# Kernel tuning notes

Hardware: AMD Instinct MI355X
Metric: run time of the kernel (lower is better)

The kernel has to match this reference:

```python
import jax, jax.numpy as jnp
import numpy as np

HIDDEN = 2048
N_HEADS = 32
N_KV = 8
HEAD_DIM = 64
B, S = 2, 2048
EPS = 1e-6
ROT_BASE = 10000.0


def _rms_norm(x, w):
    var = jnp.mean(x * x, axis=-1, keepdims=True)
    return x * jax.lax.rsqrt(var + EPS) * w


def _rotate_half(x):
    h = x.shape[-1] // 2
    return jnp.concatenate([-x[..., h:], x[..., :h]], axis=-1)


def _apply_rope(x, cos, sin):
    # x: [B,S,H,D], cos/sin: [S,D] -> broadcast over batch and heads
    c = cos[None, :, None, :]
    s = sin[None, :, None, :]
    return x * c + _rotate_half(x) * s


def setup_inputs() -> dict:
    key = jax.random.key(0)
    ks = jax.random.split(key, 12)
    sd = 0.02
    hidden_states = jax.random.normal(ks[0], (B, S, HIDDEN), dtype=jnp.float32)
    Wq = jax.random.normal(ks[1], (HIDDEN, N_HEADS * HEAD_DIM), dtype=jnp.float32) * sd
    bq = jnp.zeros((N_HEADS * HEAD_DIM,), dtype=jnp.float32)
    Wk = jax.random.normal(ks[2], (HIDDEN, N_KV * HEAD_DIM), dtype=jnp.float32) * sd
    bk = jnp.zeros((N_KV * HEAD_DIM,), dtype=jnp.float32)
    Wv = jax.random.normal(ks[3], (HIDDEN, N_KV * HEAD_DIM), dtype=jnp.float32) * sd
    bv = jnp.zeros((N_KV * HEAD_DIM,), dtype=jnp.float32)
    Wo = jax.random.normal(ks[4], (N_HEADS * HEAD_DIM, HIDDEN), dtype=jnp.float32) * sd
    bo = jnp.zeros((HIDDEN,), dtype=jnp.float32)
    qn_w = jnp.ones((HEAD_DIM,), dtype=jnp.float32)
    kn_w = jnp.ones((HEAD_DIM,), dtype=jnp.float32)
    # rotary tables (Llama convention: duplicated half-dim freqs)
    inv_freq = 1.0 / (ROT_BASE ** (np.arange(0, HEAD_DIM, 2, dtype=np.float32) / HEAD_DIM))
    t = np.arange(S, dtype=np.float32)
    freqs = np.outer(t, inv_freq)              # [S, D/2]
    emb = np.concatenate([freqs, freqs], axis=-1)  # [S, D]
    cos = jnp.asarray(np.cos(emb), dtype=jnp.float32)
    sin = jnp.asarray(np.sin(emb), dtype=jnp.float32)
    cu_seqlens = jnp.asarray([0, S, 2 * S], dtype=jnp.int32)
    return {"hidden_states": hidden_states, "Wq": Wq, "bq": bq, "Wk": Wk, "bk": bk,
            "Wv": Wv, "bv": bv, "Wo": Wo, "bo": bo, "qn_w": qn_w, "kn_w": kn_w,
            "cos": cos, "sin": sin, "cu_seqlens": cu_seqlens, "max_s": S}


def reference(hidden_states, Wq, bq, Wk, bk, Wv, bv, Wo, bo, qn_w, kn_w, cos, sin, cu_seqlens, max_s):
    b, s, _ = hidden_states.shape
    q = (hidden_states @ Wq + bq).reshape(b, s, N_HEADS, HEAD_DIM)
    k = (hidden_states @ Wk + bk).reshape(b, s, N_KV, HEAD_DIM)
    v = (hidden_states @ Wv + bv).reshape(b, s, N_KV, HEAD_DIM)
    q = _rms_norm(q, qn_w)
    k = _rms_norm(k, kn_w)
    q = _apply_rope(q, cos, sin)
    k = _apply_rope(k, cos, sin)
    # GQA: repeat_interleave kv heads to match query heads
    n_rep = N_HEADS // N_KV
    k = jnp.repeat(k, n_rep, axis=2)
    v = jnp.repeat(v, n_rep, axis=2)
    q = q.transpose(0, 2, 1, 3)  # [B,H,S,D]
    k = k.transpose(0, 2, 1, 3)
    v = v.transpose(0, 2, 1, 3)
    scale = 1.0 / jnp.sqrt(jnp.asarray(HEAD_DIM, dtype=q.dtype))
    scores = jnp.einsum("bhqd,bhkd->bhqk", q, k) * scale
    neg = jnp.finfo(scores.dtype).min
    causal = jnp.triu(jnp.ones((s, s), dtype=scores.dtype), k=1)  # [S,S]
    scores = scores + causal[None, None] * neg
    attn = jax.nn.softmax(scores, axis=-1)
    out = jnp.einsum("bhqk,bhkd->bhqd", attn, v)
    out = out.transpose(0, 2, 1, 3).reshape(b, s, N_HEADS * HEAD_DIM)
    return out @ Wo + bo
```

## Files before the change

kernel.cpp:

```cpp
#include <hip/hip_runtime.h>

typedef unsigned short u16;
typedef __attribute__((ext_vector_type(4))) float f32x4;
typedef __attribute__((ext_vector_type(16))) float f32x16;
typedef __attribute__((ext_vector_type(8))) short s16x8;
typedef __attribute__((ext_vector_type(8))) unsigned short u16x8;
typedef __attribute__((ext_vector_type(4))) unsigned short u16x4;

__device__ __forceinline__ float bf2f(u16 u) {
    union { unsigned int i; float f; } x; x.i = ((unsigned int)u) << 16; return x.f;
}
__device__ __forceinline__ u16 f2bf(float f) {
    union { float f; unsigned int i; } x; x.f = f;
    unsigned int r = x.i + 0x7FFFu + ((x.i >> 16) & 1u);
    return (u16)(r >> 16);
}
__device__ __forceinline__ void gload16(const void* g, void* l) {
    __builtin_amdgcn_global_load_lds((const __attribute__((address_space(1))) void*)g,
                                     (__attribute__((address_space(3))) void*)l, 16, 0, 0);
}
__device__ __forceinline__ unsigned cvtpk(float lo, float hi) {
    unsigned r;
    asm("v_cvt_pk_bf16_f32 %0, %1, %2" : "=v"(r) : "v"(lo), "v"(hi));
    return r;
}

#define BATCH 2
#define SEQ 2048
#define HID 2048
#define NH 32
#define NKV 8
#define HD 64
#define TOK (BATCH * SEQ)
#define NQKV 3072
#define QSCALE 0.18033688011112042f

__global__ void k_f32_to_bf16(const float* __restrict__ src, u16* __restrict__ dst, int n4) {
    int i = blockIdx.x * blockDim.x + threadIdx.x;
    if (i >= n4) return;
    f32x4 v = ((const f32x4*)src)[i];
    u16x4 o;
    o[0] = f2bf(v[0]); o[1] = f2bf(v[1]); o[2] = f2bf(v[2]); o[3] = f2bf(v[3]);
    *(u16x4*)(dst + (size_t)i * 4) = o;
}

__global__ void k_transpose_bf16(const float* __restrict__ src, u16* __restrict__ dst, int K, int N) {
    __shared__ float tile[32][33];
    int n0 = blockIdx.x * 32, k0 = blockIdx.y * 32;
    int tx = threadIdx.x, ty = threadIdx.y;
#pragma unroll
    for (int i = 0; i < 4; i++)
        tile[ty + i * 8][tx] = src[(size_t)(k0 + ty + i * 8) * N + n0 + tx];
    __syncthreads();
#pragma unroll
    for (int i = 0; i < 4; i++) {
        int n = n0 + ty + i * 8;
        dst[(size_t)n * K + k0 + tx] = f2bf(tile[tx][ty + i * 8]);
    }
}

__global__ void k_transpose_v(const u16* __restrict__ src, u16* __restrict__ dst) {
    __shared__ u16 tile[32][34];
    const u16* s = src + (size_t)blockIdx.z * SEQ * HD;
    u16* d = dst + (size_t)blockIdx.z * SEQ * HD;
    int d0 = blockIdx.x * 32;
    int s0 = blockIdx.y * 32;
    int tx = threadIdx.x, ty = threadIdx.y;
#pragma unroll
    for (int i = 0; i < 4; i++)
        tile[ty + i * 8][tx] = s[(size_t)(s0 + ty + i * 8) * HD + d0 + tx];
    __syncthreads();
#pragma unroll
    for (int i = 0; i < 4; i++)
        d[(size_t)(d0 + ty + i * 8) * SEQ + s0 + tx] = tile[tx][ty + i * 8];
}

__global__ void k_concat_bias(const float* __restrict__ bq, const float* __restrict__ bk,
                              const float* __restrict__ bv, float* __restrict__ out) {
    int i = blockIdx.x * blockDim.x + threadIdx.x;
    if (i >= NQKV) return;
    out[i] = (i < HID) ? bq[i] : (i < HID + 512 ? bk[i - HID] : bv[i - HID - 512]);
}

template <int OUT_BF16>
__global__ __launch_bounds__(256) void k_gemm_bt(const u16* __restrict__ A, const u16* __restrict__ BT,
                                                 const float* __restrict__ bias, void* __restrict__ Cout,
                                                 int M, int N, int K, int lda, int ldb) {
    __shared__ u16 As[128 * 32];
    __shared__ u16 Bs[128 * 32];
    const int t = threadIdx.x;
    const int gx = gridDim.x;
    int bid = blockIdx.y * gx + blockIdx.x;
    const int cpx = (gx * gridDim.y) >> 3;
    bid = (bid & 7) * cpx + (bid >> 3);
    const int brow = (bid / gx) * 128, bcol = (bid % gx) * 128;
    const int wid = t >> 6, lane = t & 63;
    const int wr = (wid >> 1) * 64, wc = (wid & 1) * 64;
    const int lr = lane & 15;
    const int lk = (lane >> 4) * 8;

    const int srow0 = wid * 32 + (lane >> 2);
    const int scol = (lane & 3) * 8;
    const u16* Ag0 = A + (size_t)(brow + srow0) * lda + scol;
    const u16* Ag1 = A + (size_t)(brow + srow0 + 16) * lda + scol;
    const u16* Bg0 = BT + (size_t)(bcol + srow0) * ldb + scol;
    const u16* Bg1 = BT + (size_t)(bcol + srow0 + 16) * ldb + scol;
    u16* Al0 = As + (wid * 2 + 0) * 512;
    u16* Al1 = As + (wid * 2 + 1) * 512;
    u16* Bl0 = Bs + (wid * 2 + 0) * 512;
    u16* Bl1 = Bs + (wid * 2 + 1) * 512;

    f32x4 acc[4][4] = {};
    for (int k0 = 0; k0 < K; k0 += 32) {
        __syncthreads();
        gload16(Ag0 + k0, Al0);
        gload16(Ag1 + k0, Al1);
        gload16(Bg0 + k0, Bl0);
        gload16(Bg1 + k0, Bl1);
        __syncthreads();
        s16x8 af[4], bf[4];
#pragma unroll
        for (int mi = 0; mi < 4; mi++) af[mi] = *(const s16x8*)(As + (wr + mi * 16 + lr) * 32 + lk);
#pragma unroll
        for (int ni = 0; ni < 4; ni++) bf[ni] = *(const s16x8*)(Bs + (wc + ni * 16 + lr) * 32 + lk);
#pragma unroll
        for (int mi = 0; mi < 4; mi++)
#pragma unroll
            for (int ni = 0; ni < 4; ni++)
                acc[mi][ni] = __builtin_amdgcn_mfma_f32_16x16x32_bf16(af[mi], bf[ni], acc[mi][ni], 0, 0, 0);
    }

    const int drow = ((lane >> 4) << 2);
#pragma unroll
    for (int mi = 0; mi < 4; mi++) {
#pragma unroll
        for (int ni = 0; ni < 4; ni++) {
#pragma unroll
            for (int r = 0; r < 4; r++) {
                int row = brow + wr + mi * 16 + drow + r;
                int col = bcol + wc + ni * 16 + lr;
                float v = acc[mi][ni][r] + bias[col];
                if (OUT_BF16) ((u16*)Cout)[(size_t)row * N + col] = f2bf(v);
                else          ((float*)Cout)[(size_t)row * N + col] = v;
            }
        }
    }
}

__global__ __launch_bounds__(64) void k_norm_rope(const float* __restrict__ QKV,
                                                  const float* __restrict__ qn_w, const float* __restrict__ kn_w,
                                                  const float* __restrict__ cosT, const float* __restrict__ sinT,
                                                  u16* __restrict__ Qp, u16* __restrict__ Kp, u16* __restrict__ Vp) {
    int token = blockIdx.x;
    int slot = blockIdx.y;
    int d = threadIdx.x;
    int b = token >> 11, s = token & 2047;
    const float* row = QKV + (size_t)token * NQKV;
    if (slot < 40) {
        bool isq = slot < 32;
        int h = isq ? slot : slot - 32;
        float x = isq ? row[h * HD + d] : row[HID + h * HD + d];
        float ss = x * x;
#pragma unroll
        for (int o = 32; o; o >>= 1) ss += __shfl_xor(ss, o);
        float r = rsqrtf(ss * (1.0f / 64.0f) + 1e-6f);
        float xn = x * r * (isq ? qn_w[d] : kn_w[d]);
        float part = __shfl_xor(xn, 32);
        float sign = (d < 32) ? -1.f : 1.f;
        float o = xn * cosT[s * HD + d] + sign * part * sinT[s * HD + d];
        if (isq) Qp[(((size_t)(b * NH + h) * SEQ + s) * HD) + d] = f2bf(o * QSCALE);
        else     Kp[(((size_t)(b * NKV + h) * SEQ + s) * HD) + d] = f2bf(o);
    } else {
        int h = slot - 40;
        Vp[(((size_t)(b * NKV + h) * SEQ + s) * HD) + d] = f2bf(row[HID + 512 + h * HD + d]);
    }
}

__global__ __launch_bounds__(256) void k_attn_mfma(const u16* __restrict__ Qp, const u16* __restrict__ Kp,
                                                   const u16* __restrict__ VpT, u16* __restrict__ AO) {
    __shared__ u16 K_lds[64 * 64];
    __shared__ u16 VT_lds[64 * 64];
    __shared__ u16 P_lds[4][32][76];
    const int bid = blockIdx.x;
    const int qt = 15 - (bid >> 6);
    const int hh = bid & 63;
    const int b = hh >> 5, h = hh & 31, kvh = h >> 2;
    const int t = threadIdx.x, w = t >> 6, lane = t & 63;
    const int q5 = lane & 31, hi = lane >> 5;
    const int qwb = qt * 128 + w * 32;
    const int q_abs = qwb + q5;

    const u16* Qb = Qp + (size_t)(b * NH + h) * SEQ * HD;
    const u16* Kb = Kp + (size_t)(b * NKV + kvh) * SEQ * HD;
    const u16* Vb = VpT + (size_t)(b * NKV + kvh) * HD * SEQ;

    s16x8 qf0 = *(const s16x8*)(Qb + (size_t)q_abs * HD + 0 * 16 + hi * 8);
    s16x8 qf1 = *(const s16x8*)(Qb + (size_t)q_abs * HD + 1 * 16 + hi * 8);
    s16x8 qf2 = *(const s16x8*)(Qb + (size_t)q_abs * HD + 2 * 16 + hi * 8);
    s16x8 qf3 = *(const s16x8*)(Qb + (size_t)q_abs * HD + 3 * 16 + hi * 8);

    f32x16 O0, O1;
#pragma unroll
    for (int r = 0; r < 16; r++) { O0[r] = 0.f; O1[r] = 0.f; }
    float m = -1e30f, l = 0.f;

    const int swz = (q5 & 7) << 4;
    const int nkt = 2 * (qt + 1);
    for (int kt = 0; kt < nkt; kt++) {
        const int k0 = kt * 64;
        __syncthreads();
#pragma unroll
        for (int i = 0; i < 2; i++) {
            int c = (w * 2 + i) * 64 + lane;
            int row = c >> 3, gslot = (c & 7) ^ (row & 7);
            gload16(Kb + (size_t)(k0 + row) * HD + gslot * 8, (char*)K_lds + (size_t)(w * 2 + i) * 1024);
            gload16(Vb + (size_t)row * SEQ + k0 + gslot * 8, (char*)VT_lds + (size_t)(w * 2 + i) * 1024);
        }
        __syncthreads();
        if (k0 > qwb + 31) continue;

        f32x16 s0, s1;
#pragma unroll
        for (int r = 0; r < 16; r++) { s0[r] = 0.f; s1[r] = 0.f; }
        __builtin_amdgcn_s_setprio(1);
#pragma unroll
        for (int dblk = 0; dblk < 4; dblk++) {
            s16x8 kf0 = *(const s16x8*)((const char*)K_lds + q5 * 128 + ((dblk * 32 + hi * 16) ^ swz));
            s16x8 kf1 = *(const s16x8*)((const char*)K_lds + (32 + q5) * 128 + ((dblk * 32 + hi * 16) ^ swz));
            s16x8 qq = (dblk == 0) ? qf0 : (dblk == 1) ? qf1 : (dblk == 2) ? qf2 : qf3;
            s0 = __builtin_amdgcn_mfma_f32_32x32x16_bf16(kf0, qq, s0, 0, 0, 0);
            s1 = __builtin_amdgcn_mfma_f32_32x32x16_bf16(kf1, qq, s1, 0, 0, 0);
        }
        __builtin_amdgcn_s_setprio(0);

        if (k0 + 63 > qwb) {
            const int qrel = q_abs - k0;
#pragma unroll
            for (int r = 0; r < 16; r++) {
                int kr = (r & 3) + 8 * (r >> 2) + 4 * hi;
                if (kr > qrel) s0[r] = -1e30f;
                if (kr + 32 > qrel) s1[r] = -1e30f;
            }
        }

        float mt = -1e30f;
#pragma unroll
        for (int r = 0; r < 16; r++) { mt = fmaxf(mt, s0[r]); mt = fmaxf(mt, s1[r]); }
        mt = fmaxf(mt, __shfl_xor(mt, 32));
        if (!__all(mt <= m + 8.0f)) {
            float mn = fmaxf(m, mt);
            float f = exp2f(m - mn);
            l *= f;
#pragma unroll
            for (int r = 0; r < 16; r++) { O0[r] *= f; O1[r] *= f; }
            m = mn;
        }
        float ps = 0.f;
#pragma unroll
        for (int r = 0; r < 16; r++) {
            float p0 = exp2f(s0[r] - m);
            float p1 = exp2f(s1[r] - m);
            s0[r] = p0; s1[r] = p1;
            ps += p0 + p1;
        }
        ps += __shfl_xor(ps, 32);
        l += ps;

#pragma unroll
        for (int i = 0; i < 8; i++) {
            int key = 2 * (i & 1) + 8 * (i >> 1) + 4 * hi;
            *(unsigned*)&P_lds[w][q5][key]      = cvtpk(s0[2 * i], s0[2 * i + 1]);
            *(unsigned*)&P_lds[w][q5][key + 32] = cvtpk(s1[2 * i], s1[2 * i + 1]);
        }

        __builtin_amdgcn_s_setprio(1);
#pragma unroll
        for (int ks = 0; ks < 4; ks++) {
            s16x8 pb  = *(const s16x8*)&P_lds[w][q5][ks * 16 + hi * 8];
            s16x8 vf0 = *(const s16x8*)((const char*)VT_lds + q5 * 128 + ((ks * 32 + hi * 16) ^ swz));
            s16x8 vf1 = *(const s16x8*)((const char*)VT_lds + (32 + q5) * 128 + ((ks * 32 + hi * 16) ^ swz));
            O0 = __builtin_amdgcn_mfma_f32_32x32x16_bf16(vf0, pb, O0, 0, 0, 0);
            O1 = __builtin_amdgcn_mfma_f32_32x32x16_bf16(vf1, pb, O1, 0, 0, 0);
        }
        __builtin_amdgcn_s_setprio(0);
    }

    float inv = 1.0f / l;
    u16* orow = AO + (size_t)(b * SEQ + q_abs) * (NH * HD) + h * HD;
#pragma unroll
    for (int db = 0; db < 2; db++) {
#pragma unroll
        for (int g2 = 0; g2 < 4; g2++) {
            u16x4 wv;
#pragma unroll
            for (int i2 = 0; i2 < 4; i2++) {
                float v = (db == 0 ? O0[g2 * 4 + i2] : O1[g2 * 4 + i2]) * inv;
                wv[i2] = f2bf(v);
            }
            *(u16x4*)(orow + db * 32 + g2 * 8 + hi * 4) = wv;
        }
    }
}

extern "C" void kernel_launch(void* const* d_in, const int* in_sizes, int n_in,
                              void* d_out, int out_size, void* d_ws, size_t ws_size,
                              hipStream_t stream) {
    const float* hs   = (const float*)d_in[0];
    const float* Wq   = (const float*)d_in[1];
    const float* bq   = (const float*)d_in[2];
    const float* Wk   = (const float*)d_in[3];
    const float* bk   = (const float*)d_in[4];
    const float* Wv   = (const float*)d_in[5];
    const float* bv   = (const float*)d_in[6];
    const float* Wo   = (const float*)d_in[7];
    const float* bo   = (const float*)d_in[8];
    const float* qn_w = (const float*)d_in[9];
    const float* kn_w = (const float*)d_in[10];
    const float* cosT = (const float*)d_in[11];
    const float* sinT = (const float*)d_in[12];

    char* ws = (char*)d_ws;
    size_t off = 0;
    auto alloc = [&](size_t bytes) { char* p = ws + off; off = (off + bytes + 255) & ~(size_t)255; return p; };
    u16*   Xb    = (u16*)  alloc((size_t)TOK * HID * 2);
    u16*   WTqkv = (u16*)  alloc((size_t)NQKV * HID * 2);
    u16*   WoT   = (u16*)  alloc((size_t)HID * HID * 2);
    float* bqkv  = (float*)alloc((size_t)NQKV * 4);
    float* QKV   = (float*)alloc((size_t)TOK * NQKV * 4);
    u16*   Qp    = (u16*)  alloc((size_t)BATCH * NH * SEQ * HD * 2);
    u16*   Kp    = (u16*)  alloc((size_t)BATCH * NKV * SEQ * HD * 2);
    u16*   Vp    = (u16*)  alloc((size_t)BATCH * NKV * SEQ * HD * 2);
    u16*   VpT   = (u16*)  alloc((size_t)BATCH * NKV * SEQ * HD * 2);
    u16*   AO    = (u16*)  alloc((size_t)TOK * HID * 2);
    (void)ws_size;

    k_f32_to_bf16<<<(TOK * HID / 4 + 255) / 256, 256, 0, stream>>>(hs, Xb, TOK * HID / 4);
    dim3 tb(32, 8);
    k_transpose_bf16<<<dim3(HID / 32, HID / 32), tb, 0, stream>>>(Wq, WTqkv, HID, HID);
    k_transpose_bf16<<<dim3(512 / 32, HID / 32), tb, 0, stream>>>(Wk, WTqkv + (size_t)HID * HID, HID, 512);
    k_transpose_bf16<<<dim3(512 / 32, HID / 32), tb, 0, stream>>>(Wv, WTqkv + (size_t)(HID + 512) * HID, HID, 512);
    k_transpose_bf16<<<dim3(HID / 32, HID / 32), tb, 0, stream>>>(Wo, WoT, HID, HID);
    k_concat_bias<<<(NQKV + 255) / 256, 256, 0, stream>>>(bq, bk, bv, bqkv);
    k_gemm_bt<0><<<dim3(NQKV / 128, TOK / 128), 256, 0, stream>>>(Xb, WTqkv, bqkv, QKV, TOK, NQKV, HID, HID, HID);
    k_norm_rope<<<dim3(TOK, 48), 64, 0, stream>>>(QKV, qn_w, kn_w, cosT, sinT, Qp, Kp, Vp);
    k_transpose_v<<<dim3(HD / 32, SEQ / 32, BATCH * NKV), tb, 0, stream>>>(Vp, VpT);
    k_attn_mfma<<<BATCH * NH * (SEQ / 128), 256, 0, stream>>>(Qp, Kp, VpT, AO);
    k_gemm_bt<0><<<dim3(HID / 128, TOK / 128), 256, 0, stream>>>(AO, WoT, bo, d_out, TOK, HID, HID, HID, HID);
}
```

Before: 269.4 us.

## Double-buffer K/V tiles in attention and emit QKV projection as bf16

The attention kernel now keeps two LDS buffers for K and V^T and prefetches the next key tile with async global-to-LDS loads while the current tile is computed. This cuts one of the two barriers per iteration and hides load latency behind compute. Separately, the QKV GEMM writes bf16 instead of fp32, halving intermediate traffic into the norm/rope kernel. The bf16 rounding happens before the RMS norm, which slightly lowers precision, and the extra LDS buffers may reduce occupancy.

```diff
diff --git a/kernel.cpp b/kernel.cpp
--- a/kernel.cpp
+++ b/kernel.cpp
@@ -147,7 +147,7 @@
     }
 }
 
-__global__ __launch_bounds__(64) void k_norm_rope(const float* __restrict__ QKV,
+__global__ __launch_bounds__(64) void k_norm_rope(const u16* __restrict__ QKV,
                                                   const float* __restrict__ qn_w, const float* __restrict__ kn_w,
                                                   const float* __restrict__ cosT, const float* __restrict__ sinT,
                                                   u16* __restrict__ Qp, u16* __restrict__ Kp, u16* __restrict__ Vp) {
@@ -155,11 +155,11 @@
     int slot = blockIdx.y;
     int d = threadIdx.x;
     int b = token >> 11, s = token & 2047;
-    const float* row = QKV + (size_t)token * NQKV;
+    const u16* row = QKV + (size_t)token * NQKV;
     if (slot < 40) {
         bool isq = slot < 32;
         int h = isq ? slot : slot - 32;
-        float x = isq ? row[h * HD + d] : row[HID + h * HD + d];
+        float x = isq ? bf2f(row[h * HD + d]) : bf2f(row[HID + h * HD + d]);
         float ss = x * x;
 #pragma unroll
         for (int o = 32; o; o >>= 1) ss += __shfl_xor(ss, o);
@@ -172,14 +172,14 @@
         else     Kp[(((size_t)(b * NKV + h) * SEQ + s) * HD) + d] = f2bf(o);
     } else {
         int h = slot - 40;
-        Vp[(((size_t)(b * NKV + h) * SEQ + s) * HD) + d] = f2bf(row[HID + 512 + h * HD + d]);
+        Vp[(((size_t)(b * NKV + h) * SEQ + s) * HD) + d] = row[HID + 512 + h * HD + d];
     }
 }
 
 __global__ __launch_bounds__(256) void k_attn_mfma(const u16* __restrict__ Qp, const u16* __restrict__ Kp,
                                                    const u16* __restrict__ VpT, u16* __restrict__ AO) {
-    __shared__ u16 K_lds[64 * 64];
-    __shared__ u16 VT_lds[64 * 64];
+    __shared__ u16 K_lds[2][64 * 64];
+    __shared__ u16 VT_lds[2][64 * 64];
     __shared__ u16 P_lds[4][32][76];
     const int bid = blockIdx.x;
     const int qt = 15 - (bid >> 6);
@@ -194,6 +194,10 @@
     const u16* Kb = Kp + (size_t)(b * NKV + kvh) * SEQ * HD;
     const u16* Vb = VpT + (size_t)(b * NKV + kvh) * HD * SEQ;
 
+    const int c0 = (w * 2 + 0) * 64 + lane, c1 = (w * 2 + 1) * 64 + lane;
+    const int r0 = c0 >> 3, g0 = (c0 & 7) ^ (r0 & 7);
+    const int r1 = c1 >> 3, g1 = (c1 & 7) ^ (r1 & 7);
+
     s16x8 qf0 = *(const s16x8*)(Qb + (size_t)q_abs * HD + 0 * 16 + hi * 8);
     s16x8 qf1 = *(const s16x8*)(Qb + (size_t)q_abs * HD + 1 * 16 + hi * 8);
     s16x8 qf2 = *(const s16x8*)(Qb + (size_t)q_abs * HD + 2 * 16 + hi * 8);
@@ -206,83 +210,97 @@
 
     const int swz = (q5 & 7) << 4;
     const int nkt = 2 * (qt + 1);
+
+    {
+        gload16(Kb + (size_t)r0 * HD + g0 * 8, (char*)K_lds[0] + (size_t)(w * 2 + 0) * 1024);
+        gload16(Kb + (size_t)r1 * HD + g1 * 8, (char*)K_lds[0] + (size_t)(w * 2 + 1) * 1024);
+        gload16(Vb + (size_t)r0 * SEQ + g0 * 8, (char*)VT_lds[0] + (size_t)(w * 2 + 0) * 1024);
+        gload16(Vb + (size_t)r1 * SEQ + g1 * 8, (char*)VT_lds[0] + (size_t)(w * 2 + 1) * 1024);
+    }
+    __syncthreads();
+
     for (int kt = 0; kt < nkt; kt++) {
         const int k0 = kt * 64;
+        const int cur = kt & 1;
+        if (kt + 1 < nkt) {
+            const int nk0 = k0 + 64;
+            gload16(Kb + (size_t)(nk0 + r0) * HD + g0 * 8, (char*)K_lds[cur ^ 1] + (size_t)(w * 2 + 0) * 1024);
+            gload16(Kb + (size_t)(nk0 + r1) * HD + g1 * 8, (char*)K_lds[cur ^ 1] + (size_t)(w * 2 + 1) * 1024);
+            gload16(Vb + (size_t)r0 * SEQ + nk0 + g0 * 8, (char*)VT_lds[cur ^ 1] + (size_t)(w * 2 + 0) * 1024);
+            gload16(Vb + (size_t)r1 * SEQ + nk0 + g1 * 8, (char*)VT_lds[cur ^ 1] + (size_t)(w * 2 + 1) * 1024);
+        }
+
+        if (k0 <= qwb + 31) {
+            const char* Kc = (const char*)K_lds[cur];
+            const char* Vc = (const char*)VT_lds[cur];
+
+            f32x16 s0, s1;
+#pragma unroll
+            for (int r = 0; r < 16; r++) { s0[r] = 0.f; s1[r] = 0.f; }
+            __builtin_amdgcn_s_setprio(1);
+#pragma unroll
+            for (int dblk = 0; dblk < 4; dblk++) {
+                s16x8 kf0 = *(const s16x8*)(Kc + q5 * 128 + ((dblk * 32 + hi * 16) ^ swz));
+                s16x8 kf1 = *(const s16x8*)(Kc + (32 + q5) * 128 + ((dblk * 32 + hi * 16) ^ swz));
+                s16x8 qq = (dblk == 0) ? qf0 : (dblk == 1) ? qf1 : (dblk == 2) ? qf2 : qf3;
+                s0 = __builtin_amdgcn_mfma_f32_32x32x16_bf16(kf0, qq, s0, 0, 0, 0);
+                s1 = __builtin_amdgcn_mfma_f32_32x32x16_bf16(kf1, qq, s1, 0, 0, 0);
+            }
+            __builtin_amdgcn_s_setprio(0);
+
+            if (k0 + 63 > qwb) {
+                const int qrel = q_abs - k0;
+#pragma unroll
+                for (int r = 0; r < 16; r++) {
+                    int kr = (r & 3) + 8 * (r >> 2) + 4 * hi;
+                    if (kr > qrel) s0[r] = -1e30f;
+                    if (kr + 32 > qrel) s1[r] = -1e30f;
+                }
+            }
+
+            float mt = -1e30f;
+#pragma unroll
+            for (int r = 0; r < 16; r++) { mt = fmaxf(mt, s0[r]); mt = fmaxf(mt, s1[r]); }
+            mt = fmaxf(mt, __shfl_xor(mt, 32));
+            if (!__all(mt <= m + 8.0f)) {
+                float mn = fmaxf(m, mt);
+                float f = exp2f(m - mn);
+                l *= f;
+#pragma unroll
+                for (int r = 0; r < 16; r++) { O0[r] *= f; O1[r] *= f; }
+                m = mn;
+            }
+            float ps = 0.f;
+#pragma unroll
+            for (int r = 0; r < 16; r++) {
+                float p0 = exp2f(s0[r] - m);
+                float p1 = exp2f(s1[r] - m);
+                s0[r] = p0; s1[r] = p1;
+                ps += p0 + p1;
+            }
+            ps += __shfl_xor(ps, 32);
+            l += ps;
+
+#pragma unroll
+            for (int i = 0; i < 8; i++) {
+                int key = 2 * (i & 1) + 8 * (i >> 1) + 4 * hi;
+                *(unsigned*)&P_lds[w][q5][key]      = cvtpk(s0[2 * i], s0[2 * i + 1]);
+                *(unsigned*)&P_lds[w][q5][key + 32] = cvtpk(s1[2 * i], s1[2 * i + 1]);
+            }
+
+            __builtin_amdgcn_s_setprio(1);
+#pragma unroll
+            for (int ks = 0; ks < 4; ks++) {
+                s16x8 pb  = *(const s16x8*)&P_lds[w][q5][ks * 16 + hi * 8];
+                s16x8 vf0 = *(const s16x8*)(Vc + q5 * 128 + ((ks * 32 + hi * 16) ^ swz));
+                s16x8 vf1 = *(const s16x8*)(Vc + (32 + q5) * 128 + ((ks * 32 + hi * 16) ^ swz));
+                O0 = __builtin_amdgcn_mfma_f32_32x32x16_bf16(vf0, pb, O0, 0, 0, 0);
+                O1 = __builtin_amdgcn_mfma_f32_32x32x16_bf16(vf1, pb, O1, 0, 0, 0);
+            }
+            __builtin_amdgcn_s_setprio(0);
+        }
+
         __syncthreads();
-#pragma unroll
-        for (int i = 0; i < 2; i++) {
-            int c = (w * 2 + i) * 64 + lane;
-            int row = c >> 3, gslot = (c & 7) ^ (row & 7);
-            gload16(Kb + (size_t)(k0 + row) * HD + gslot * 8, (char*)K_lds + (size_t)(w * 2 + i) * 1024);
-            gload16(Vb + (size_t)row * SEQ + k0 + gslot * 8, (char*)VT_lds + (size_t)(w * 2 + i) * 1024);
-        }
-        __syncthreads();
-        if (k0 > qwb + 31) continue;
-
-        f32x16 s0, s1;
-#pragma unroll
-        for (int r = 0; r < 16; r++) { s0[r] = 0.f; s1[r] = 0.f; }
-        __builtin_amdgcn_s_setprio(1);
-#pragma unroll
-        for (int dblk = 0; dblk < 4; dblk++) {
-            s16x8 kf0 = *(const s16x8*)((const char*)K_lds + q5 * 128 + ((dblk * 32 + hi * 16) ^ swz));
-            s16x8 kf1 = *(const s16x8*)((const char*)K_lds + (32 + q5) * 128 + ((dblk * 32 + hi * 16) ^ swz));
-            s16x8 qq = (dblk == 0) ? qf0 : (dblk == 1) ? qf1 : (dblk == 2) ? qf2 : qf3;
-            s0 = __builtin_amdgcn_mfma_f32_32x32x16_bf16(kf0, qq, s0, 0, 0, 0);
-            s1 = __builtin_amdgcn_mfma_f32_32x32x16_bf16(kf1, qq, s1, 0, 0, 0);
-        }
-        __builtin_amdgcn_s_setprio(0);
-
-        if (k0 + 63 > qwb) {
-            const int qrel = q_abs - k0;
-#pragma unroll
-            for (int r = 0; r < 16; r++) {
-                int kr = (r & 3) + 8 * (r >> 2) + 4 * hi;
-                if (kr > qrel) s0[r] = -1e30f;
-                if (kr + 32 > qrel) s1[r] = -1e30f;
-            }
-        }
-
-        float mt = -1e30f;
-#pragma unroll
-        for (int r = 0; r < 16; r++) { mt = fmaxf(mt, s0[r]); mt = fmaxf(mt, s1[r]); }
-        mt = fmaxf(mt, __shfl_xor(mt, 32));
-        if (!__all(mt <= m + 8.0f)) {
-            float mn = fmaxf(m, mt);
-            float f = exp2f(m - mn);
-            l *= f;
-#pragma unroll
-            for (int r = 0; r < 16; r++) { O0[r] *= f; O1[r] *= f; }
-            m = mn;
-        }
-        float ps = 0.f;
-#pragma unroll
-        for (int r = 0; r < 16; r++) {
-            float p0 = exp2f(s0[r] - m);
-            float p1 = exp2f(s1[r] - m);
-            s0[r] = p0; s1[r] = p1;
-            ps += p0 + p1;
-        }
-        ps += __shfl_xor(ps, 32);
-        l += ps;
-
-#pragma unroll
-        for (int i = 0; i < 8; i++) {
-            int key = 2 * (i & 1) + 8 * (i >> 1) + 4 * hi;
-            *(unsigned*)&P_lds[w][q5][key]      = cvtpk(s0[2 * i], s0[2 * i + 1]);
-            *(unsigned*)&P_lds[w][q5][key + 32] = cvtpk(s1[2 * i], s1[2 * i + 1]);
-        }
-
-        __builtin_amdgcn_s_setprio(1);
-#pragma unroll
-        for (int ks = 0; ks < 4; ks++) {
-            s16x8 pb  = *(const s16x8*)&P_lds[w][q5][ks * 16 + hi * 8];
-            s16x8 vf0 = *(const s16x8*)((const char*)VT_lds + q5 * 128 + ((ks * 32 + hi * 16) ^ swz));
-            s16x8 vf1 = *(const s16x8*)((const char*)VT_lds + (32 + q5) * 128 + ((ks * 32 + hi * 16) ^ swz));
-            O0 = __builtin_amdgcn_mfma_f32_32x32x16_bf16(vf0, pb, O0, 0, 0, 0);
-            O1 = __builtin_amdgcn_mfma_f32_32x32x16_bf16(vf1, pb, O1, 0, 0, 0);
-        }
-        __builtin_amdgcn_s_setprio(0);
     }
 
     float inv = 1.0f / l;
@@ -326,7 +344,7 @@
     u16*   WTqkv = (u16*)  alloc((size_t)NQKV * HID * 2);
     u16*   WoT   = (u16*)  alloc((size_t)HID * HID * 2);
     float* bqkv  = (float*)alloc((size_t)NQKV * 4);
-    float* QKV   = (float*)alloc((size_t)TOK * NQKV * 4);
+    u16*   QKV   = (u16*)  alloc((size_t)TOK * NQKV * 2);
     u16*   Qp    = (u16*)  alloc((size_t)BATCH * NH * SEQ * HD * 2);
     u16*   Kp    = (u16*)  alloc((size_t)BATCH * NKV * SEQ * HD * 2);
     u16*   Vp    = (u16*)  alloc((size_t)BATCH * NKV * SEQ * HD * 2);
@@ -341,7 +359,7 @@
     k_transpose_bf16<<<dim3(512 / 32, HID / 32), tb, 0, stream>>>(Wv, WTqkv + (size_t)(HID + 512) * HID, HID, 512);
     k_transpose_bf16<<<dim3(HID / 32, HID / 32), tb, 0, stream>>>(Wo, WoT, HID, HID);
     k_concat_bias<<<(NQKV + 255) / 256, 256, 0, stream>>>(bq, bk, bv, bqkv);
-    k_gemm_bt<0><<<dim3(NQKV / 128, TOK / 128), 256, 0, stream>>>(Xb, WTqkv, bqkv, QKV, TOK, NQKV, HID, HID, HID);
+    k_gemm_bt<1><<<dim3(NQKV / 128, TOK / 128), 256, 0, stream>>>(Xb, WTqkv, bqkv, QKV, TOK, NQKV, HID, HID, HID);
     k_norm_rope<<<dim3(TOK, 48), 64, 0, stream>>>(QKV, qn_w, kn_w, cosT, sinT, Qp, Kp, Vp);
     k_transpose_v<<<dim3(HD / 32, SEQ / 32, BATCH * NKV), tb, 0, stream>>>(Vp, VpT);
     k_attn_mfma<<<BATCH * NH * (SEQ / 128), 256, 0, stream>>>(Qp, Kp, VpT, AO);
```

New measurement: 269.9 us. No clear change (+0.2%).

## Emit bf16 QKV from GEMM and load K/V fragments directly from global in attention

Applied to the files above, without the earlier changes.

The QKV projection GEMM now writes bf16 instead of fp32, halving the intermediate write and the read in the norm/rope kernel, and V is copied through without conversion. The attention kernel drops its shared-memory K/V staging and block-wide barriers. Each wave now loads its own K and V MFMA fragments straight from global memory and runs its own causal trip count. This removes synchronisation and lets waves skip fully masked tiles, at the cost of redundant global/L2 traffic across the four waves and exposed load latency without prefetching. Rounding QKV to bf16 before RMS norm also slightly lowers precision.

```diff
diff --git a/kernel.cpp b/kernel.cpp
--- a/kernel.cpp
+++ b/kernel.cpp
@@ -147,7 +147,7 @@
     }
 }
 
-__global__ __launch_bounds__(64) void k_norm_rope(const float* __restrict__ QKV,
+__global__ __launch_bounds__(64) void k_norm_rope(const u16* __restrict__ QKV,
                                                   const float* __restrict__ qn_w, const float* __restrict__ kn_w,
                                                   const float* __restrict__ cosT, const float* __restrict__ sinT,
                                                   u16* __restrict__ Qp, u16* __restrict__ Kp, u16* __restrict__ Vp) {
@@ -155,11 +155,11 @@
     int slot = blockIdx.y;
     int d = threadIdx.x;
     int b = token >> 11, s = token & 2047;
-    const float* row = QKV + (size_t)token * NQKV;
+    const u16* row = QKV + (size_t)token * NQKV;
     if (slot < 40) {
         bool isq = slot < 32;
         int h = isq ? slot : slot - 32;
-        float x = isq ? row[h * HD + d] : row[HID + h * HD + d];
+        float x = isq ? bf2f(row[h * HD + d]) : bf2f(row[HID + h * HD + d]);
         float ss = x * x;
 #pragma unroll
         for (int o = 32; o; o >>= 1) ss += __shfl_xor(ss, o);
@@ -172,14 +172,12 @@
         else     Kp[(((size_t)(b * NKV + h) * SEQ + s) * HD) + d] = f2bf(o);
     } else {
         int h = slot - 40;
-        Vp[(((size_t)(b * NKV + h) * SEQ + s) * HD) + d] = f2bf(row[HID + 512 + h * HD + d]);
+        Vp[(((size_t)(b * NKV + h) * SEQ + s) * HD) + d] = row[HID + 512 + h * HD + d];
     }
 }
 
 __global__ __launch_bounds__(256) void k_attn_mfma(const u16* __restrict__ Qp, const u16* __restrict__ Kp,
                                                    const u16* __restrict__ VpT, u16* __restrict__ AO) {
-    __shared__ u16 K_lds[64 * 64];
-    __shared__ u16 VT_lds[64 * 64];
     __shared__ u16 P_lds[4][32][76];
     const int bid = blockIdx.x;
     const int qt = 15 - (bid >> 6);
@@ -204,20 +202,27 @@
     for (int r = 0; r < 16; r++) { O0[r] = 0.f; O1[r] = 0.f; }
     float m = -1e30f, l = 0.f;
 
-    const int swz = (q5 & 7) << 4;
-    const int nkt = 2 * (qt + 1);
-    for (int kt = 0; kt < nkt; kt++) {
+    const u16* Krow0 = Kb + (size_t)q5 * HD + hi * 8;
+    const u16* Krow1 = Kb + (size_t)(32 + q5) * HD + hi * 8;
+    const u16* Vrow0 = Vb + (size_t)q5 * SEQ + hi * 8;
+    const u16* Vrow1 = Vb + (size_t)(32 + q5) * SEQ + hi * 8;
+
+    const int nkt_w = 2 * qt + 1 + (w >> 1);
+    for (int kt = 0; kt < nkt_w; kt++) {
         const int k0 = kt * 64;
-        __syncthreads();
-#pragma unroll
-        for (int i = 0; i < 2; i++) {
-            int c = (w * 2 + i) * 64 + lane;
-            int row = c >> 3, gslot = (c & 7) ^ (row & 7);
-            gload16(Kb + (size_t)(k0 + row) * HD + gslot * 8, (char*)K_lds + (size_t)(w * 2 + i) * 1024);
-            gload16(Vb + (size_t)row * SEQ + k0 + gslot * 8, (char*)VT_lds + (size_t)(w * 2 + i) * 1024);
-        }
-        __syncthreads();
-        if (k0 > qwb + 31) continue;
+
+        s16x8 kf0[4], kf1[4];
+#pragma unroll
+        for (int dblk = 0; dblk < 4; dblk++) {
+            kf0[dblk] = *(const s16x8*)(Krow0 + (size_t)k0 * HD + dblk * 16);
+            kf1[dblk] = *(const s16x8*)(Krow1 + (size_t)k0 * HD + dblk * 16);
+        }
+        s16x8 vf0[4], vf1[4];
+#pragma unroll
+        for (int ks = 0; ks < 4; ks++) {
+            vf0[ks] = *(const s16x8*)(Vrow0 + k0 + ks * 16);
+            vf1[ks] = *(const s16x8*)(Vrow1 + k0 + ks * 16);
+        }
 
         f32x16 s0, s1;
 #pragma unroll
@@ -225,11 +230,9 @@
         __builtin_amdgcn_s_setprio(1);
 #pragma unroll
         for (int dblk = 0; dblk < 4; dblk++) {
-            s16x8 kf0 = *(const s16x8*)((const char*)K_lds + q5 * 128 + ((dblk * 32 + hi * 16) ^ swz));
-            s16x8 kf1 = *(const s16x8*)((const char*)K_lds + (32 + q5) * 128 + ((dblk * 32 + hi * 16) ^ swz));
             s16x8 qq = (dblk == 0) ? qf0 : (dblk == 1) ? qf1 : (dblk == 2) ? qf2 : qf3;
-            s0 = __builtin_amdgcn_mfma_f32_32x32x16_bf16(kf0, qq, s0, 0, 0, 0);
-            s1 = __builtin_amdgcn_mfma_f32_32x32x16_bf16(kf1, qq, s1, 0, 0, 0);
+            s0 = __builtin_amdgcn_mfma_f32_32x32x16_bf16(kf0[dblk], qq, s0, 0, 0, 0);
+            s1 = __builtin_amdgcn_mfma_f32_32x32x16_bf16(kf1[dblk], qq, s1, 0, 0, 0);
         }
         __builtin_amdgcn_s_setprio(0);
 
@@ -276,11 +279,9 @@
         __builtin_amdgcn_s_setprio(1);
 #pragma unroll
         for (int ks = 0; ks < 4; ks++) {
-            s16x8 pb  = *(const s16x8*)&P_lds[w][q5][ks * 16 + hi * 8];
-            s16x8 vf0 = *(const s16x8*)((const char*)VT_lds + q5 * 128 + ((ks * 32 + hi * 16) ^ swz));
-            s16x8 vf1 = *(const s16x8*)((const char*)VT_lds + (32 + q5) * 128 + ((ks * 32 + hi * 16) ^ swz));
-            O0 = __builtin_amdgcn_mfma_f32_32x32x16_bf16(vf0, pb, O0, 0, 0, 0);
-            O1 = __builtin_amdgcn_mfma_f32_32x32x16_bf16(vf1, pb, O1, 0, 0, 0);
+            s16x8 pb = *(const s16x8*)&P_lds[w][q5][ks * 16 + hi * 8];
+            O0 = __builtin_amdgcn_mfma_f32_32x32x16_bf16(vf0[ks], pb, O0, 0, 0, 0);
+            O1 = __builtin_amdgcn_mfma_f32_32x32x16_bf16(vf1[ks], pb, O1, 0, 0, 0);
         }
         __builtin_amdgcn_s_setprio(0);
     }
@@ -326,7 +327,7 @@
     u16*   WTqkv = (u16*)  alloc((size_t)NQKV * HID * 2);
     u16*   WoT   = (u16*)  alloc((size_t)HID * HID * 2);
     float* bqkv  = (float*)alloc((size_t)NQKV * 4);
-    float* QKV   = (float*)alloc((size_t)TOK * NQKV * 4);
+    u16*   QKV   = (u16*)  alloc((size_t)TOK * NQKV * 2);
     u16*   Qp    = (u16*)  alloc((size_t)BATCH * NH * SEQ * HD * 2);
     u16*   Kp    = (u16*)  alloc((size_t)BATCH * NKV * SEQ * HD * 2);
     u16*   Vp    = (u16*)  alloc((size_t)BATCH * NKV * SEQ * HD * 2);
@@ -341,7 +342,7 @@
     k_transpose_bf16<<<dim3(512 / 32, HID / 32), tb, 0, stream>>>(Wv, WTqkv + (size_t)(HID + 512) * HID, HID, 512);
     k_transpose_bf16<<<dim3(HID / 32, HID / 32), tb, 0, stream>>>(Wo, WoT, HID, HID);
     k_concat_bias<<<(NQKV + 255) / 256, 256, 0, stream>>>(bq, bk, bv, bqkv);
-    k_gemm_bt<0><<<dim3(NQKV / 128, TOK / 128), 256, 0, stream>>>(Xb, WTqkv, bqkv, QKV, TOK, NQKV, HID, HID, HID);
+    k_gemm_bt<1><<<dim3(NQKV / 128, TOK / 128), 256, 0, stream>>>(Xb, WTqkv, bqkv, QKV, TOK, NQKV, HID, HID, HID);
     k_norm_rope<<<dim3(TOK, 48), 64, 0, stream>>>(QKV, qn_w, kn_w, cosT, sinT, Qp, Kp, Vp);
     k_transpose_v<<<dim3(HD / 32, SEQ / 32, BATCH * NKV), tb, 0, stream>>>(Vp, VpT);
     k_attn_mfma<<<BATCH * NH * (SEQ / 128), 256, 0, stream>>>(Qp, Kp, VpT, AO);
```

Result: slower. 321.2 us (+19.2%).

## Use 256x256-tile QKV GEMM with bf16 output and batch norm-rope heads per block

Applied to the files above, without the earlier changes.

Replaces the 128x128 QKV projection GEMM with a new 512-thread kernel that computes 256x256 tiles. It double-buffers LDS with direct global-to-LDS loads, uses an XOR swizzle and a grid remap across XCDs, and raises wave priority around the MFMA block. The QKV intermediate is now stored as bf16 instead of fp32, which halves the write and read traffic into the norm/rope kernel. That kernel now handles four heads per 256-thread block. The cost is lower precision before the RMS norm and a kernel that assumes the dimensions divide evenly by 256.

```diff
diff --git a/kernel.cpp b/kernel.cpp
--- a/kernel.cpp
+++ b/kernel.cpp
@@ -147,19 +147,122 @@
     }
 }
 
-__global__ __launch_bounds__(64) void k_norm_rope(const float* __restrict__ QKV,
-                                                  const float* __restrict__ qn_w, const float* __restrict__ kn_w,
-                                                  const float* __restrict__ cosT, const float* __restrict__ sinT,
-                                                  u16* __restrict__ Qp, u16* __restrict__ Kp, u16* __restrict__ Vp) {
+template <int OUT_BF16>
+__global__ __launch_bounds__(512, 1) void k_gemm256(const u16* __restrict__ A, const u16* __restrict__ BT,
+                                                    const float* __restrict__ bias, void* __restrict__ Cout,
+                                                    int gxn, int K, int lda, int ldb, int N) {
+    __shared__ u16 LDS[2][2][256 * 64];
+    const int tid = threadIdx.x;
+    const int w = tid >> 6, lane = tid & 63;
+    const int wm = w >> 2, wn = w & 3;
+    const int lr = lane & 15, g = lane >> 4;
+    const int nwg = gridDim.x;
+    int bid = blockIdx.x;
+    const int cpx = nwg >> 3;
+    bid = (bid & 7) * cpx + (bid >> 3);
+    const int brow = (bid / gxn) * 256, bcol = (bid % gxn) * 256;
+
+    const int lrow8 = lane >> 3;
+    const int gs = (lane & 7) ^ lrow8;
+    const u16* Ag[4]; const u16* Bg[4];
+#pragma unroll
+    for (int p = 0; p < 4; p++) {
+        int row = (w * 4 + p) * 8 + lrow8;
+        Ag[p] = A + (size_t)(brow + row) * lda + gs * 8;
+        Bg[p] = BT + (size_t)(bcol + row) * ldb + gs * 8;
+    }
+
+    f32x4 acc[8][4] = {};
+
+#pragma unroll
+    for (int p = 0; p < 4; p++) {
+        gload16(Ag[p], &LDS[0][0][(w * 4 + p) * 512]);
+        gload16(Bg[p], &LDS[0][1][(w * 4 + p) * 512]);
+    }
+    asm volatile("s_waitcnt vmcnt(0)" ::: "memory");
+    __builtin_amdgcn_s_barrier();
+    asm volatile("" ::: "memory");
+
+    const int NT = K >> 6;
+    int cur = 0;
+    for (int tk = 0; tk < NT; tk++) {
+        const u16* Al = &LDS[cur][0][0];
+        const u16* Bl = &LDS[cur][1][0];
+        u16* An = &LDS[cur ^ 1][0][0];
+        u16* Bn = &LDS[cur ^ 1][1][0];
+        const int knext = (tk + 1) << 6;
+        const bool pf = (tk + 1 < NT);
+        s16x8 bfr[4][2];
+#pragma unroll
+        for (int p = 0; p < 4; p++) {
+            s16x8 af[2][2];
+#pragma unroll
+            for (int j = 0; j < 2; j++) {
+                const char* rowp = (const char*)Al + (size_t)(wm * 128 + (2 * p + j) * 16 + lr) * 128;
+#pragma unroll
+                for (int kk = 0; kk < 2; kk++)
+                    af[j][kk] = *(const s16x8*)(rowp + (((kk * 4 + g) ^ (lr & 7)) << 4));
+            }
+            if (p == 0) {
+#pragma unroll
+                for (int ni = 0; ni < 4; ni++) {
+                    const char* rowp = (const char*)Bl + (size_t)(wn * 64 + ni * 16 + lr) * 128;
+#pragma unroll
+                    for (int kk = 0; kk < 2; kk++)
+                        bfr[ni][kk] = *(const s16x8*)(rowp + (((kk * 4 + g) ^ (lr & 7)) << 4));
+                }
+            }
+            if (pf) {
+                gload16(Ag[p] + knext, &An[(w * 4 + p) * 512]);
+                gload16(Bg[p] + knext, &Bn[(w * 4 + p) * 512]);
+            }
+            __builtin_amdgcn_s_barrier();
+            __builtin_amdgcn_s_setprio(1);
+#pragma unroll
+            for (int j = 0; j < 2; j++)
+#pragma unroll
+                for (int ni = 0; ni < 4; ni++) {
+                    acc[2 * p + j][ni] = __builtin_amdgcn_mfma_f32_16x16x32_bf16(af[j][0], bfr[ni][0], acc[2 * p + j][ni], 0, 0, 0);
+                    acc[2 * p + j][ni] = __builtin_amdgcn_mfma_f32_16x16x32_bf16(af[j][1], bfr[ni][1], acc[2 * p + j][ni], 0, 0, 0);
+                }
+            __builtin_amdgcn_s_setprio(0);
+            __builtin_amdgcn_s_barrier();
+        }
+        if (pf) asm volatile("s_waitcnt vmcnt(0)" ::: "memory");
+        __builtin_amdgcn_s_barrier();
+        asm volatile("" ::: "memory");
+        cur ^= 1;
+    }
+
+#pragma unroll
+    for (int mi = 0; mi < 8; mi++) {
+#pragma unroll
+        for (int ni = 0; ni < 4; ni++) {
+#pragma unroll
+            for (int r = 0; r < 4; r++) {
+                int row = brow + wm * 128 + mi * 16 + g * 4 + r;
+                int col = bcol + wn * 64 + ni * 16 + lr;
+                float v = acc[mi][ni][r] + bias[col];
+                if (OUT_BF16) ((u16*)Cout)[(size_t)row * N + col] = f2bf(v);
+                else          ((float*)Cout)[(size_t)row * N + col] = v;
+            }
+        }
+    }
+}
+
+__global__ __launch_bounds__(256) void k_norm_rope(const u16* __restrict__ QKV,
+                                                   const float* __restrict__ qn_w, const float* __restrict__ kn_w,
+                                                   const float* __restrict__ cosT, const float* __restrict__ sinT,
+                                                   u16* __restrict__ Qp, u16* __restrict__ Kp, u16* __restrict__ Vp) {
     int token = blockIdx.x;
-    int slot = blockIdx.y;
-    int d = threadIdx.x;
+    int slot = blockIdx.y * 4 + (threadIdx.x >> 6);
+    int d = threadIdx.x & 63;
     int b = token >> 11, s = token & 2047;
-    const float* row = QKV + (size_t)token * NQKV;
+    const u16* row = QKV + (size_t)token * NQKV;
     if (slot < 40) {
         bool isq = slot < 32;
         int h = isq ? slot : slot - 32;
-        float x = isq ? row[h * HD + d] : row[HID + h * HD + d];
+        float x = isq ? bf2f(row[h * HD + d]) : bf2f(row[HID + h * HD + d]);
         float ss = x * x;
 #pragma unroll
         for (int o = 32; o; o >>= 1) ss += __shfl_xor(ss, o);
@@ -172,7 +275,7 @@
         else     Kp[(((size_t)(b * NKV + h) * SEQ + s) * HD) + d] = f2bf(o);
     } else {
         int h = slot - 40;
-        Vp[(((size_t)(b * NKV + h) * SEQ + s) * HD) + d] = f2bf(row[HID + 512 + h * HD + d]);
+        Vp[(((size_t)(b * NKV + h) * SEQ + s) * HD) + d] = row[HID + 512 + h * HD + d];
     }
 }
 
@@ -326,7 +429,7 @@
     u16*   WTqkv = (u16*)  alloc((size_t)NQKV * HID * 2);
     u16*   WoT   = (u16*)  alloc((size_t)HID * HID * 2);
     float* bqkv  = (float*)alloc((size_t)NQKV * 4);
-    float* QKV   = (float*)alloc((size_t)TOK * NQKV * 4);
+    u16*   QKV   = (u16*)  alloc((size_t)TOK * NQKV * 2);
     u16*   Qp    = (u16*)  alloc((size_t)BATCH * NH * SEQ * HD * 2);
     u16*   Kp    = (u16*)  alloc((size_t)BATCH * NKV * SEQ * HD * 2);
     u16*   Vp    = (u16*)  alloc((size_t)BATCH * NKV * SEQ * HD * 2);
@@ -341,8 +444,9 @@
     k_transpose_bf16<<<dim3(512 / 32, HID / 32), tb, 0, stream>>>(Wv, WTqkv + (size_t)(HID + 512) * HID, HID, 512);
     k_transpose_bf16<<<dim3(HID / 32, HID / 32), tb, 0, stream>>>(Wo, WoT, HID, HID);
     k_concat_bias<<<(NQKV + 255) / 256, 256, 0, stream>>>(bq, bk, bv, bqkv);
-    k_gemm_bt<0><<<dim3(NQKV / 128, TOK / 128), 256, 0, stream>>>(Xb, WTqkv, bqkv, QKV, TOK, NQKV, HID, HID, HID);
-    k_norm_rope<<<dim3(TOK, 48), 64, 0, stream>>>(QKV, qn_w, kn_w, cosT, sinT, Qp, Kp, Vp);
+    k_gemm256<1><<<dim3((TOK / 256) * (NQKV / 256)), 512, 0, stream>>>(Xb, WTqkv, bqkv, QKV,
+                                                                        NQKV / 256, HID, HID, HID, NQKV);
+    k_norm_rope<<<dim3(TOK, 12), 256, 0, stream>>>(QKV, qn_w, kn_w, cosT, sinT, Qp, Kp, Vp);
     k_transpose_v<<<dim3(HD / 32, SEQ / 32, BATCH * NKV), tb, 0, stream>>>(Vp, VpT);
     k_attn_mfma<<<BATCH * NH * (SEQ / 128), 256, 0, stream>>>(Qp, Kp, VpT, AO);
     k_gemm_bt<0><<<dim3(HID / 128, TOK / 128), 256, 0, stream>>>(AO, WoT, bo, d_out, TOK, HID, HID, HID, HID);
```

Measured after the change: 250.1 us. 7.2% less time.
